# Kernel tuning notes

Measured on AMD Instinct MI355X. Metric: run time of the kernel, lower is better.

The kernel has to match this reference:

```python
import jax, jax.numpy as jnp
import numpy as np

B, T = 256, 511          # batch, seq_len (512 - 1)
V = 128                  # tune_vocab_size
RV, MV, KV = 30, 20, 40  # rhythm/meter/key vocab sizes
E, ET = 16, 32           # context emb dim, tune emb dim
D = 3 * E + ET           # 80, LSTM input dim
H = 256                  # LSTM hidden


def setup_inputs() -> dict:
    key = jax.random.key(0)
    ks = jax.random.split(key, 14)
    s = 0.05
    return {
        "tune": jax.random.randint(ks[0], (B, T), 0, V + 1, dtype=jnp.int32),
        "rhythm": jax.random.randint(ks[1], (B, 1), 0, RV + 1, dtype=jnp.int32),
        "meter": jax.random.randint(ks[2], (B, 1), 0, MV + 1, dtype=jnp.int32),
        "key": jax.random.randint(ks[3], (B, 1), 0, KV + 1, dtype=jnp.int32),
        "tune_length": jax.random.randint(ks[4], (B, 1), 1, T, dtype=jnp.int32),
        # learned parameters
        "emb_rhythm": jax.random.normal(ks[5], (RV + 1, E), jnp.float32) * s,
        "emb_meter": jax.random.normal(ks[6], (MV + 1, E), jnp.float32) * s,
        "emb_key": jax.random.normal(ks[7], (KV + 1, E), jnp.float32) * s,
        "emb_tune": jax.random.normal(ks[8], (V + 1, ET), jnp.float32) * s,
        "W": jax.random.normal(ks[9], (D, 4 * H), jnp.float32) * s,   # input kernel (gates i,f,c,o)
        "U": jax.random.normal(ks[10], (H, 4 * H), jnp.float32) * s,  # recurrent kernel
        "b": jax.random.normal(ks[11], (4 * H,), jnp.float32) * s,
        "Wd": jax.random.normal(ks[12], (H, V), jnp.float32) * s,     # output dense
        "bd": jax.random.normal(ks[13], (V,), jnp.float32) * s,
    }


def reference(tune, rhythm, meter, key, tune_length,
              emb_rhythm, emb_meter, emb_key, emb_tune, W, U, b, Wd, bd):
    Bc, Tc = tune.shape
    Hc = U.shape[0]
    # conditioning context, repeated over time: [B, 48]
    ctx = jnp.concatenate(
        [emb_rhythm[rhythm[:, 0]], emb_meter[meter[:, 0]], emb_key[key[:, 0]]], axis=-1)
    # full LSTM input: [B, T, 80]
    x = jnp.concatenate(
        [jnp.broadcast_to(ctx[:, None, :], (Bc, Tc, ctx.shape[-1])), emb_tune[tune]], axis=-1)
    # sequence mask: step t valid iff t < tune_length  -> [B, T]
    mask = jnp.arange(Tc, dtype=tune_length.dtype)[None, :] < tune_length

    xs = jnp.swapaxes(x, 0, 1)   # [T, B, 80]
    ms = mask.T                  # [T, B]

    def step(carry, inp):
        h, c = carry
        xt, mt = inp
        z = xt @ W + h @ U + b                      # [B, 4H]
        i, f, g, o = jnp.split(z, 4, axis=-1)       # keras gate order i,f,c,o
        i = jax.nn.sigmoid(i)
        f = jax.nn.sigmoid(f)
        g = jnp.tanh(g)
        o = jax.nn.sigmoid(o)
        c_new = f * c + i * g
        h_new = o * jnp.tanh(c_new)
        m = mt[:, None]
        # masked steps: carry state through unchanged, output zeros
        h2 = jnp.where(m, h_new, h)
        c2 = jnp.where(m, c_new, c)
        out = jnp.where(m, h_new, jnp.zeros_like(h_new))
        return (h2, c2), out

    init = (jnp.zeros((Bc, Hc), x.dtype), jnp.zeros((Bc, Hc), x.dtype))
    _, ys = jax.lax.scan(step, init, (xs, ms))  # ys: [T, B, H]
    ys = jnp.swapaxes(ys, 0, 1)                 # [B, T, H]
    return ys @ Wd + bd                         # logits [B, T, V]
```

## Files before the change

### kernel.cpp

```cpp
#include <hip/hip_runtime.h>
#include <hip/hip_fp16.h>
#include <stdint.h>

#define BB 256
#define TT 511
#define VV 128
#define HH 256
#define G4 1024

typedef _Float16 h2_t __attribute__((ext_vector_type(2)));

__device__ __forceinline__ float fdot2(uint32_t a, uint32_t b, float c) {
  return __builtin_amdgcn_fdot2(__builtin_bit_cast(h2_t, a),
                                __builtin_bit_cast(h2_t, b), c, false);
}

__device__ __forceinline__ uint32_t pack2(float a, float b) {
  __half ha = __float2half(a), hb = __float2half(b);
  return (uint32_t)__half_as_ushort(ha) | ((uint32_t)__half_as_ushort(hb) << 16);
}


__global__ __launch_bounds__(1024) void prep_ctx_k(
    const int* __restrict__ rhythm, const int* __restrict__ meter, const int* __restrict__ keyi,
    const float* __restrict__ er, const float* __restrict__ em, const float* __restrict__ ek,
    const float* __restrict__ W, const float* __restrict__ bias, float* __restrict__ ctxW) {
  int b = blockIdx.x, j = threadIdx.x;
  int r = rhythm[b], m = meter[b], k = keyi[b];
  float acc = bias[j];
#pragma unroll
  for (int e = 0; e < 16; e++) acc += er[r*16+e] * W[(0+e)*G4 + j];
#pragma unroll
  for (int e = 0; e < 16; e++) acc += em[m*16+e] * W[(16+e)*G4 + j];
#pragma unroll
  for (int e = 0; e < 16; e++) acc += ek[k*16+e] * W[(32+e)*G4 + j];
  ctxW[b*G4 + j] = acc;
}

__global__ __launch_bounds__(1024) void prep_tune_k(
    const float* __restrict__ et, const float* __restrict__ W, float* __restrict__ tuneW) {
  int v = blockIdx.x, j = threadIdx.x;
  float acc = 0.f;
#pragma unroll
  for (int e = 0; e < 32; e++) acc += et[v*32+e] * W[(48+e)*G4 + j];
  tuneW[v*G4 + j] = acc;
}

__global__ __launch_bounds__(1024) void prep_U_k(
    const float* __restrict__ U, uint32_t* __restrict__ Up) {
  int kk = blockIdx.x, j = threadIdx.x;
  Up[kk*G4 + j] = pack2(U[(2*kk)*G4 + j], U[(2*kk+1)*G4 + j]);
}

__global__ __launch_bounds__(128) void prep_Wd_k(
    const float* __restrict__ Wd, uint32_t* __restrict__ Wdp) {
  int kp = blockIdx.x, v = threadIdx.x;
  Wdp[kp*VV + v] = pack2(Wd[(2*kp)*VV + v], Wd[(2*kp+1)*VV + v]);
}


#define NT 512
#define KREG 48
#define KLDS 16
#define ULDS_ROWS (2*KLDS)
#define OFF_ZPART (ULDS_ROWS*G4)
#define OFF_CTX   (OFF_ZPART + 2*G4)
#define OFF_HBUF  (OFF_CTX + G4)
#define OFF_TLDS  (OFF_HBUF + 128)
#define SMEM_U32  (OFF_TLDS + 512)
#define SMEM_BYTES (SMEM_U32*4)

__global__ __launch_bounds__(NT, 2) void lstm_rec_k(
    const int* __restrict__ tune, const int* __restrict__ tlen,
    const uint32_t* __restrict__ Up, const float* __restrict__ ctxW,
    const float* __restrict__ tuneW, __half* __restrict__ h_hist) {
  extern __shared__ uint32_t smem[];
  uint32_t* Ulds   = smem;
  float*    zpart  = (float*)(smem + OFF_ZPART);
  float*    ctxlds = (float*)(smem + OFF_CTX);
  uint32_t* hbuf   = smem + OFF_HBUF;
  int*      tlds   = (int*)(smem + OFF_TLDS);

  int b    = blockIdx.x;
  int tid  = threadIdx.x;
  int g    = tid >> 8;
  int q    = tid & 255;
  int lane = tid & 63;
  int L    = tlen[b];

  for (int i = tid; i < TT; i += NT) tlds[i] = tune[b*TT + i];
  for (int i = tid; i < G4; i += NT) ctxlds[i] = ctxW[b*G4 + i];
  if (tid < 128) hbuf[tid] = 0u;
  for (int idx = tid; idx < ULDS_ROWS*G4; idx += NT) {
    int row = idx >> 10, j = idx & 1023;
    int gg = row / KLDS, r = row % KLDS;
    Ulds[idx] = Up[(gg*64 + KREG + r)*G4 + j];
  }

  uint4 ureg[KREG];
  {
    const uint32_t* ubase = Up + (size_t)(g*64)*G4 + 4*q;
#pragma unroll
    for (int kk = 0; kk < KREG; kk++) ureg[kk] = *(const uint4*)(ubase + (size_t)kk*G4);
  }
  float cc = 0.f;
  __syncthreads();

  const uint32_t* uldsrow = Ulds + (size_t)(g*KLDS)*G4 + 4*q;
  __half* hh_base = h_hist + (size_t)b*TT*HH;

  for (int t = 0; t < L; t++) {
    uint32_t vh = hbuf[g*64 + lane];
    int v = tlds[t];
    float tw0, tw1, tw2, tw3;
    if (tid < HH) {
      const float* twp = tuneW + (size_t)v*G4 + tid;
      tw0 = twp[0]; tw1 = twp[256]; tw2 = twp[512]; tw3 = twp[768];
    }
    float a0e = 0.f, a1e = 0.f, a2e = 0.f, a3e = 0.f;
    float a0o = 0.f, a1o = 0.f, a2o = 0.f, a3o = 0.f;
#pragma unroll
    for (int kk = 0; kk < KREG; kk += 2) {
      uint32_t hs0 = (uint32_t)__builtin_amdgcn_readlane((int)vh, kk);
      uint32_t hs1 = (uint32_t)__builtin_amdgcn_readlane((int)vh, kk + 1);
      a0e = fdot2(hs0, ureg[kk].x, a0e);
      a1e = fdot2(hs0, ureg[kk].y, a1e);
      a2e = fdot2(hs0, ureg[kk].z, a2e);
      a3e = fdot2(hs0, ureg[kk].w, a3e);
      a0o = fdot2(hs1, ureg[kk+1].x, a0o);
      a1o = fdot2(hs1, ureg[kk+1].y, a1o);
      a2o = fdot2(hs1, ureg[kk+1].z, a2o);
      a3o = fdot2(hs1, ureg[kk+1].w, a3o);
    }
#pragma unroll
    for (int r = 0; r < KLDS; r += 2) {
      uint4 ua = *(const uint4*)(uldsrow + (size_t)r*G4);
      uint4 ub = *(const uint4*)(uldsrow + (size_t)(r+1)*G4);
      uint32_t hs0 = (uint32_t)__builtin_amdgcn_readlane((int)vh, KREG + r);
      uint32_t hs1 = (uint32_t)__builtin_amdgcn_readlane((int)vh, KREG + r + 1);
      a0e = fdot2(hs0, ua.x, a0e);
      a1e = fdot2(hs0, ua.y, a1e);
      a2e = fdot2(hs0, ua.z, a2e);
      a3e = fdot2(hs0, ua.w, a3e);
      a0o = fdot2(hs1, ub.x, a0o);
      a1o = fdot2(hs1, ub.y, a1o);
      a2o = fdot2(hs1, ub.z, a2o);
      a3o = fdot2(hs1, ub.w, a3o);
    }
    *(float4*)(zpart + g*G4 + 4*q) =
        make_float4(a0e + a0o, a1e + a1o, a2e + a2o, a3e + a3o);
    __syncthreads();
    if (tid < HH) {
      float zi = zpart[tid      ] + zpart[G4 + tid      ] + ctxlds[tid      ] + tw0;
      float zf = zpart[tid + 256] + zpart[G4 + tid + 256] + ctxlds[tid + 256] + tw1;
      float zg = zpart[tid + 512] + zpart[G4 + tid + 512] + ctxlds[tid + 512] + tw2;
      float zo = zpart[tid + 768] + zpart[G4 + tid + 768] + ctxlds[tid + 768] + tw3;
      float gi = 1.f / (1.f + __expf(-zi));
      float gf = 1.f / (1.f + __expf(-zf));
      float e2 = __expf(2.f*zg);
      float gg = (e2 - 1.f) / (e2 + 1.f);
      float go = 1.f / (1.f + __expf(-zo));
      cc = gf*cc + gi*gg;
      float ec = __expf(2.f*cc);
      float th = (ec - 1.f) / (ec + 1.f);
      float hv = go * th;
      __half hhv = __float2half(hv);
      ((__half*)hbuf)[tid] = hhv;
      hh_base[(size_t)t*HH + tid] = hhv;
    }
    __syncthreads();
  }
}


__global__ __launch_bounds__(256) void out_gemm_k(
    const uint32_t* __restrict__ hsrc, const uint32_t* __restrict__ Wdp,
    const float* __restrict__ bd, const int* __restrict__ tlen,
    float* __restrict__ out) {
  __shared__ uint32_t A[64][128];
  int bb = blockIdx.x;
  int b  = bb >> 3, t0 = (bb & 7) << 6;
  int tid = threadIdx.x;
  int L = tlen[b];
  for (int idx = tid; idx < 64*128; idx += 256) {
    int r = idx >> 7, kp = idx & 127;
    int t = t0 + r;
    A[r][kp] = (t < TT) ? hsrc[((size_t)b*TT + t)*128 + kp] : 0u;
  }
  __syncthreads();
  int v = tid & 127, rg = tid >> 7;
  float acc[32];
#pragma unroll
  for (int r = 0; r < 32; r++) acc[r] = 0.f;
  for (int kb = 0; kb < 4; kb++) {
    uint32_t w[32];
#pragma unroll
    for (int q = 0; q < 32; q++) w[q] = Wdp[(kb*32+q)*VV + v];
#pragma unroll
    for (int r = 0; r < 32; r++) {
      const uint32_t* ar = &A[rg*32 + r][kb*32];
#pragma unroll
      for (int q4 = 0; q4 < 8; q4++) {
        uint4 a4 = *(const uint4*)(ar + q4*4);
        acc[r] = fdot2(a4.x, w[4*q4+0], acc[r]);
        acc[r] = fdot2(a4.y, w[4*q4+1], acc[r]);
        acc[r] = fdot2(a4.z, w[4*q4+2], acc[r]);
        acc[r] = fdot2(a4.w, w[4*q4+3], acc[r]);
      }
    }
  }
  float bias = bd[v];
#pragma unroll
  for (int r = 0; r < 32; r++) {
    int t = t0 + rg*32 + r;
    if (t < TT) {
      out[((size_t)b*TT + t)*VV + v] = (t < L) ? (acc[r] + bias) : bias;
    }
  }
}


extern "C" void kernel_launch(void* const* d_in, const int* in_sizes, int n_in,
                              void* d_out, int out_size, void* d_ws, size_t ws_size,
                              hipStream_t stream) {
  const int*   tune   = (const int*)d_in[0];
  const int*   rhythm = (const int*)d_in[1];
  const int*   meter  = (const int*)d_in[2];
  const int*   keyi   = (const int*)d_in[3];
  const int*   tlen   = (const int*)d_in[4];
  const float* er     = (const float*)d_in[5];
  const float* em     = (const float*)d_in[6];
  const float* ek     = (const float*)d_in[7];
  const float* et     = (const float*)d_in[8];
  const float* W      = (const float*)d_in[9];
  const float* U      = (const float*)d_in[10];
  const float* bias   = (const float*)d_in[11];
  const float* Wd     = (const float*)d_in[12];
  const float* bd     = (const float*)d_in[13];
  (void)in_sizes; (void)n_in; (void)out_size; (void)ws_size;

  char* ws = (char*)d_ws;
  uint32_t* Up    = (uint32_t*)(ws);
  float*    ctxW  = (float*)(ws + (512<<10));
  float*    tuneW = (float*)(ws + (512<<10) + (1024<<10));
  uint32_t* Wdp   = (uint32_t*)(ws + (512<<10) + (1024<<10) + (516<<10));

  hipFuncSetAttribute((const void*)lstm_rec_k,
                      hipFuncAttributeMaxDynamicSharedMemorySize, SMEM_BYTES);

  prep_ctx_k <<<BB,    1024, 0, stream>>>(rhythm, meter, keyi, er, em, ek, W, bias, ctxW);
  prep_tune_k<<<VV+1,  1024, 0, stream>>>(et, W, tuneW);
  prep_U_k   <<<128,   1024, 0, stream>>>(U, Up);
  prep_Wd_k  <<<128,   VV,   0, stream>>>(Wd, Wdp);
  lstm_rec_k <<<BB, NT, SMEM_BYTES, stream>>>(tune, tlen, Up, ctxW, tuneW, (__half*)d_out);
  out_gemm_k <<<BB*8,  256,  0, stream>>>((const uint32_t*)d_out, Wdp, bd, tlen, (float*)d_out);
}
```

Before: 1.033 ms.

## Interleave gate columns so each thread owns one hidden unit's four gates

Permutes the gate-column layout of U, the context projection and the tune projection so that thread q's four output columns are the i,f,c,o gates of hidden unit q. Both thread groups then compute the full gate nonlinearity redundantly from their own partial sum plus the other group's partial read from LDS, and only the owning group writes h. This removes the single-group tail phase and the LDS context buffer, loads tuneW and ctx as float4, and shifts the register/LDS split of U from 48/16 to 50/14 rows. The cost is more register pressure and duplicated activation math.

```diff
diff --git a/kernel.cpp b/kernel.cpp
--- a/kernel.cpp
+++ b/kernel.cpp
@@ -21,35 +21,39 @@
 }
 
 
+
 __global__ __launch_bounds__(1024) void prep_ctx_k(
     const int* __restrict__ rhythm, const int* __restrict__ meter, const int* __restrict__ keyi,
     const float* __restrict__ er, const float* __restrict__ em, const float* __restrict__ ek,
     const float* __restrict__ W, const float* __restrict__ bias, float* __restrict__ ctxW) {
-  int b = blockIdx.x, j = threadIdx.x;
+  int b = blockIdx.x, p = threadIdx.x;
+  int c = (p >> 2) + 256 * (p & 3);
   int r = rhythm[b], m = meter[b], k = keyi[b];
-  float acc = bias[j];
-#pragma unroll
-  for (int e = 0; e < 16; e++) acc += er[r*16+e] * W[(0+e)*G4 + j];
-#pragma unroll
-  for (int e = 0; e < 16; e++) acc += em[m*16+e] * W[(16+e)*G4 + j];
-#pragma unroll
-  for (int e = 0; e < 16; e++) acc += ek[k*16+e] * W[(32+e)*G4 + j];
-  ctxW[b*G4 + j] = acc;
+  float acc = bias[c];
+#pragma unroll
+  for (int e = 0; e < 16; e++) acc += er[r*16+e] * W[(0+e)*G4 + c];
+#pragma unroll
+  for (int e = 0; e < 16; e++) acc += em[m*16+e] * W[(16+e)*G4 + c];
+#pragma unroll
+  for (int e = 0; e < 16; e++) acc += ek[k*16+e] * W[(32+e)*G4 + c];
+  ctxW[b*G4 + p] = acc;
 }
 
 __global__ __launch_bounds__(1024) void prep_tune_k(
     const float* __restrict__ et, const float* __restrict__ W, float* __restrict__ tuneW) {
-  int v = blockIdx.x, j = threadIdx.x;
+  int v = blockIdx.x, p = threadIdx.x;
+  int c = (p >> 2) + 256 * (p & 3);
   float acc = 0.f;
 #pragma unroll
-  for (int e = 0; e < 32; e++) acc += et[v*32+e] * W[(48+e)*G4 + j];
-  tuneW[v*G4 + j] = acc;
+  for (int e = 0; e < 32; e++) acc += et[v*32+e] * W[(48+e)*G4 + c];
+  tuneW[v*G4 + p] = acc;
 }
 
 __global__ __launch_bounds__(1024) void prep_U_k(
     const float* __restrict__ U, uint32_t* __restrict__ Up) {
-  int kk = blockIdx.x, j = threadIdx.x;
-  Up[kk*G4 + j] = pack2(U[(2*kk)*G4 + j], U[(2*kk+1)*G4 + j]);
+  int kk = blockIdx.x, p = threadIdx.x;
+  int c = (p >> 2) + 256 * (p & 3);
+  Up[kk*G4 + p] = pack2(U[(2*kk)*G4 + c], U[(2*kk+1)*G4 + c]);
 }
 
 __global__ __launch_bounds__(128) void prep_Wd_k(
@@ -60,14 +64,12 @@
 
 
 #define NT 512
-#define KREG 48
-#define KLDS 16
-#define ULDS_ROWS (2*KLDS)
-#define OFF_ZPART (ULDS_ROWS*G4)
-#define OFF_CTX   (OFF_ZPART + 2*G4)
-#define OFF_HBUF  (OFF_CTX + G4)
+#define KREG 50
+#define KLDS 14
+#define OFF_ZPART (2*KLDS*G4)
+#define OFF_HBUF  (OFF_ZPART + 2*G4)
 #define OFF_TLDS  (OFF_HBUF + 128)
-#define SMEM_U32  (OFF_TLDS + 512)
+#define SMEM_U32  (OFF_TLDS + TT + 1)
 #define SMEM_BYTES (SMEM_U32*4)
 
 __global__ __launch_bounds__(NT, 2) void lstm_rec_k(
@@ -75,11 +77,10 @@
     const uint32_t* __restrict__ Up, const float* __restrict__ ctxW,
     const float* __restrict__ tuneW, __half* __restrict__ h_hist) {
   extern __shared__ uint32_t smem[];
-  uint32_t* Ulds   = smem;
-  float*    zpart  = (float*)(smem + OFF_ZPART);
-  float*    ctxlds = (float*)(smem + OFF_CTX);
-  uint32_t* hbuf   = smem + OFF_HBUF;
-  int*      tlds   = (int*)(smem + OFF_TLDS);
+  uint32_t* Ulds  = smem;
+  float*    zpart = (float*)(smem + OFF_ZPART);
+  uint32_t* hbuf  = smem + OFF_HBUF;
+  int*      tlds  = (int*)(smem + OFF_TLDS);
 
   int b    = blockIdx.x;
   int tid  = threadIdx.x;
@@ -89,12 +90,11 @@
   int L    = tlen[b];
 
   for (int i = tid; i < TT; i += NT) tlds[i] = tune[b*TT + i];
-  for (int i = tid; i < G4; i += NT) ctxlds[i] = ctxW[b*G4 + i];
   if (tid < 128) hbuf[tid] = 0u;
-  for (int idx = tid; idx < ULDS_ROWS*G4; idx += NT) {
-    int row = idx >> 10, j = idx & 1023;
+  for (int idx = tid; idx < 2*KLDS*G4; idx += NT) {
+    int row = idx >> 10, p = idx & 1023;
     int gg = row / KLDS, r = row % KLDS;
-    Ulds[idx] = Up[(gg*64 + KREG + r)*G4 + j];
+    Ulds[idx] = Up[(gg*64 + KREG + r)*G4 + p];
   }
 
   uint4 ureg[KREG];
@@ -103,20 +103,19 @@
 #pragma unroll
     for (int kk = 0; kk < KREG; kk++) ureg[kk] = *(const uint4*)(ubase + (size_t)kk*G4);
   }
+  float4 ctxv = *(const float4*)(ctxW + (size_t)b*G4 + 4*q);
   float cc = 0.f;
   __syncthreads();
 
   const uint32_t* uldsrow = Ulds + (size_t)(g*KLDS)*G4 + 4*q;
-  __half* hh_base = h_hist + (size_t)b*TT*HH;
+  bool owner = ((q >> 7) == g);
+  __half* hh_base = h_hist + (size_t)b*TT*HH + q;
 
   for (int t = 0; t < L; t++) {
     uint32_t vh = hbuf[g*64 + lane];
     int v = tlds[t];
-    float tw0, tw1, tw2, tw3;
-    if (tid < HH) {
-      const float* twp = tuneW + (size_t)v*G4 + tid;
-      tw0 = twp[0]; tw1 = twp[256]; tw2 = twp[512]; tw3 = twp[768];
-    }
+    float4 tw = *(const float4*)(tuneW + (size_t)v*G4 + 4*q);
+
     float a0e = 0.f, a1e = 0.f, a2e = 0.f, a3e = 0.f;
     float a0o = 0.f, a1o = 0.f, a2o = 0.f, a3o = 0.f;
 #pragma unroll
@@ -147,26 +146,28 @@
       a2o = fdot2(hs1, ub.z, a2o);
       a3o = fdot2(hs1, ub.w, a3o);
     }
-    *(float4*)(zpart + g*G4 + 4*q) =
-        make_float4(a0e + a0o, a1e + a1o, a2e + a2o, a3e + a3o);
+    float s0 = a0e + a0o, s1 = a1e + a1o, s2 = a2e + a2o, s3 = a3e + a3o;
+    *(float4*)(zpart + g*G4 + 4*q) = make_float4(s0, s1, s2, s3);
     __syncthreads();
-    if (tid < HH) {
-      float zi = zpart[tid      ] + zpart[G4 + tid      ] + ctxlds[tid      ] + tw0;
-      float zf = zpart[tid + 256] + zpart[G4 + tid + 256] + ctxlds[tid + 256] + tw1;
-      float zg = zpart[tid + 512] + zpart[G4 + tid + 512] + ctxlds[tid + 512] + tw2;
-      float zo = zpart[tid + 768] + zpart[G4 + tid + 768] + ctxlds[tid + 768] + tw3;
-      float gi = 1.f / (1.f + __expf(-zi));
-      float gf = 1.f / (1.f + __expf(-zf));
-      float e2 = __expf(2.f*zg);
-      float gg = (e2 - 1.f) / (e2 + 1.f);
-      float go = 1.f / (1.f + __expf(-zo));
-      cc = gf*cc + gi*gg;
-      float ec = __expf(2.f*cc);
-      float th = (ec - 1.f) / (ec + 1.f);
-      float hv = go * th;
+
+    float4 zp = *(const float4*)(zpart + (1-g)*G4 + 4*q);
+    float zi = s0 + zp.x + ctxv.x + tw.x;
+    float zf = s1 + zp.y + ctxv.y + tw.y;
+    float zg = s2 + zp.z + ctxv.z + tw.z;
+    float zo = s3 + zp.w + ctxv.w + tw.w;
+    float gi = 1.f / (1.f + __expf(-zi));
+    float gf = 1.f / (1.f + __expf(-zf));
+    float e2 = __expf(2.f*zg);
+    float gg = (e2 - 1.f) / (e2 + 1.f);
+    float go = 1.f / (1.f + __expf(-zo));
+    cc = gf*cc + gi*gg;
+    float ec = __expf(2.f*cc);
+    float th = (ec - 1.f) / (ec + 1.f);
+    float hv = go * th;
+    if (owner) {
       __half hhv = __float2half(hv);
-      ((__half*)hbuf)[tid] = hhv;
-      hh_base[(size_t)t*HH + tid] = hhv;
+      ((__half*)hbuf)[q] = hhv;
+      hh_base[(size_t)t*HH] = hhv;
     }
     __syncthreads();
   }
```

Measured after the change: 1.059 ms. 1.03x slower.
